# Kernel optimization log

Measured on AMD Instinct MI355X. Metric: run time of the kernel, lower is better.

Reference implementation:

```python
import jax, jax.numpy as jnp
import numpy as np


def setup_inputs() -> dict:
    key = jax.random.key(0)
    k1, k2 = jax.random.split(key)
    inputs = jax.random.normal(k1, (4, 8, 24, 24, 64), dtype=jnp.float32)
    gamma = jax.random.normal(k2, (1,), dtype=jnp.float32)
    return {"inputs": inputs, "gamma": gamma}


def reference(inputs, gamma):
    # inputs: (B, D, H, W, C); flatten spatial dims to N = D*H*W
    B, D, H, W, C = inputs.shape
    N = D * H * W
    q = inputs.reshape(B, N, C)                       # proj_query (B, N, C)
    # energy = Q @ Q^T -> (B, N, N)
    energy = jnp.einsum('bnc,bmc->bnm', q, q)
    attention = jax.nn.softmax(energy, axis=-1)       # softmax over last axis
    out = jnp.einsum('bnm,bmc->bnc', attention, q)    # (B, N, C)
    out = out.reshape(B, D, H, W, C)
    return gamma * out + inputs
```

## Files before the change

### kernel.cpp

```cpp
#include <hip/hip_runtime.h>

typedef __bf16 bf16_t;
typedef bf16_t bf16x8 __attribute__((ext_vector_type(8)));
typedef float  f32x4  __attribute__((ext_vector_type(4)));
typedef unsigned int u32;
typedef u32    u32x4  __attribute__((ext_vector_type(4)));
typedef unsigned short u16;

#define B_SZ   4
#define N_SZ   4608
#define C_SZ   64
#define KVB    32
#define QROWS  32
#define NKVT   (N_SZ / KVB)
#define NQT    (N_SZ / QROWS)
#define WV     4
#define TPW    (NKVT / WV)

__device__ __forceinline__ f32x4 mfma16(bf16x8 a, bf16x8 b, f32x4 c) {
  return __builtin_amdgcn_mfma_f32_16x16x32_bf16(a, b, c, 0, 0, 0);
}

__device__ __forceinline__ u32 pk2(float a, float b) {
  u16 ua = __builtin_bit_cast(u16, (bf16_t)a);
  u16 ub = __builtin_bit_cast(u16, (bf16_t)b);
  return (u32)ua | ((u32)ub << 16);
}

__global__ __launch_bounds__(256) void transform_k(
    const float* __restrict__ in, bf16_t* __restrict__ khi,
    bf16_t* __restrict__ klo, bf16_t* __restrict__ vt) {
  __shared__ float tile[64 * 65];
  const int bid = blockIdx.x;
  const int b  = bid / 72;
  const int n0 = (bid - b * 72) * 64;
  const int t  = threadIdx.x;
  {
    const int nl = t >> 2, c0 = (t & 3) * 16;
    const float* src = in + ((size_t)(b * N_SZ + n0 + nl)) * C_SZ + c0;
    float v[16];
    *(float4*)(v +  0) = *(const float4*)(src +  0);
    *(float4*)(v +  4) = *(const float4*)(src +  4);
    *(float4*)(v +  8) = *(const float4*)(src +  8);
    *(float4*)(v + 12) = *(const float4*)(src + 12);
    bf16x8 h8[2], l8[2];
#pragma unroll
    for (int i = 0; i < 16; ++i) {
      bf16_t h = (bf16_t)v[i];
      h8[i >> 3][i & 7] = h;
      l8[i >> 3][i & 7] = (bf16_t)(v[i] - (float)h);
      tile[nl * 65 + c0 + i] = v[i];
    }
    bf16_t* dh = khi + ((size_t)(b * N_SZ + n0 + nl)) * C_SZ + c0;
    bf16_t* dl = klo + ((size_t)(b * N_SZ + n0 + nl)) * C_SZ + c0;
    *(bf16x8*)(dh) = h8[0]; *(bf16x8*)(dh + 8) = h8[1];
    *(bf16x8*)(dl) = l8[0]; *(bf16x8*)(dl + 8) = l8[1];
  }
  __syncthreads();
  {
    const int c = t >> 2, m0 = (t & 3) * 16;
    bf16x8 o[2];
#pragma unroll
    for (int i = 0; i < 16; ++i)
      o[i >> 3][i & 7] = (bf16_t)tile[(m0 + i) * 65 + c];
    bf16_t* dst = vt + ((size_t)(b * C_SZ + c)) * N_SZ + n0 + m0;
    *(bf16x8*)(dst) = o[0]; *(bf16x8*)(dst + 8) = o[1];
  }
}

#define LOAD_TILE(KV0, KH, KL, VF)                                             \
  {                                                                            \
    _Pragma("unroll")                                                          \
    for (int ct = 0; ct < 2; ++ct)                                             \
      _Pragma("unroll")                                                        \
      for (int ks = 0; ks < 2; ++ks) {                                         \
        const size_t a = (size_t)((KV0) + ct * 16 + c15) * C_SZ + ks * 32 + g * 8; \
        KH[ct][ks] = *(const bf16x8*)(kh_b + a);                               \
        KL[ct][ks] = *(const bf16x8*)(kl_b + a);                               \
      }                                                                        \
    _Pragma("unroll")                                                          \
    for (int co = 0; co < 4; ++co)                                             \
      VF[co] = *(const bf16x8*)(vt_b + (size_t)(co * 16 + c15) * N_SZ + (KV0) + g * 8); \
  }

__global__ __launch_bounds__(256, 2) void attn_fwd(
    const float* __restrict__ in, const bf16_t* __restrict__ khi,
    const bf16_t* __restrict__ klo, const bf16_t* __restrict__ vt,
    const float* __restrict__ gamma_p, float* __restrict__ out) {
  __shared__ float obuf[256 * 36];
  __shared__ float mlbuf[4 * 2 * 2 * 16];

  const int bid0 = blockIdx.x;
  const int bid  = (bid0 & 7) * 72 + (bid0 >> 3);
  const int b  = bid / NQT;
  const int qt = bid - b * NQT;
  const int t  = threadIdx.x;
  const int w  = t >> 6, l = t & 63;
  const int c15 = l & 15, g = l >> 4;

  const bf16_t* kh_b = khi + (size_t)b * N_SZ * C_SZ;
  const bf16_t* kl_b = klo + (size_t)b * N_SZ * C_SZ;
  const bf16_t* vt_b = vt  + (size_t)b * C_SZ * N_SZ;

  bf16x8 qh[2][2], ql[2][2];
#pragma unroll
  for (int j = 0; j < 2; ++j)
#pragma unroll
    for (int ks = 0; ks < 2; ++ks) {
      const size_t a = (size_t)(qt * QROWS + j * 16 + c15) * C_SZ + ks * 32 + g * 8;
      qh[j][ks] = *(const bf16x8*)(kh_b + a);
      ql[j][ks] = *(const bf16x8*)(kl_b + a);
    }

  f32x4 acc[4][2];
#pragma unroll
  for (int co = 0; co < 4; ++co)
#pragma unroll
    for (int j = 0; j < 2; ++j)
      acc[co][j] = (f32x4){0.f, 0.f, 0.f, 0.f};
  float m_j[2] = {-3.0e38f, -3.0e38f}, l_j[2] = {0.f, 0.f};

  const int sA = ((l >> 4) & 1) * 32 + c15;
  const int sB = sA + 16;
  const bool hi_half = (l >= 32);

  bf16x8 khf[2][2], klf[2][2], vf[4];
  LOAD_TILE(w * KVB, khf, klf, vf);

  for (int it = 0; it < TPW; ++it) {
    const int itn = (it + 1 < TPW) ? it + 1 : 0;
    const int kvn = (w + itn * WV) * KVB;
    bf16x8 nkh[2][2], nkl[2][2], nvf[4];
    LOAD_TILE(kvn, nkh, nkl, nvf);

    f32x4 s[2][2];
#pragma unroll
    for (int j = 0; j < 2; ++j)
#pragma unroll
      for (int ct = 0; ct < 2; ++ct) {
        f32x4 a = (f32x4){0.f, 0.f, 0.f, 0.f};
#pragma unroll
        for (int ks = 0; ks < 2; ++ks) {
          a = mfma16(khf[ct][ks], qh[j][ks], a);
          a = mfma16(khf[ct][ks], ql[j][ks], a);
          a = mfma16(klf[ct][ks], qh[j][ks], a);
        }
        s[j][ct] = a;
      }

#pragma unroll
    for (int j = 0; j < 2; ++j) {
      float mx = fmaxf(fmaxf(fmaxf(s[j][0][0], s[j][0][1]), fmaxf(s[j][0][2], s[j][0][3])),
                       fmaxf(fmaxf(s[j][1][0], s[j][1][1]), fmaxf(s[j][1][2], s[j][1][3])));
      mx = fmaxf(mx, __shfl_xor(mx, 16, 64));
      mx = fmaxf(mx, __shfl_xor(mx, 32, 64));
      const float mn = fmaxf(m_j[j], mx);
      const float sc = __expf(m_j[j] - mn);
      m_j[j] = mn;
      float rs = 0.f;
#pragma unroll
      for (int ct = 0; ct < 2; ++ct)
#pragma unroll
        for (int r = 0; r < 4; ++r) {
          const float e = __expf(s[j][ct][r] - mn);
          s[j][ct][r] = e;
          rs += e;
        }
      rs += __shfl_xor(rs, 16, 64);
      rs += __shfl_xor(rs, 32, 64);
      l_j[j] = l_j[j] * sc + rs;
#pragma unroll
      for (int co = 0; co < 4; ++co)
        acc[co][j] *= sc;

      const u32 L0 = pk2(s[j][0][0], s[j][0][1]);
      const u32 H0 = pk2(s[j][0][2], s[j][0][3]);
      const u32 L1 = pk2(s[j][1][0], s[j][1][1]);
      const u32 H1 = pk2(s[j][1][2], s[j][1][3]);
      const u32 aL0 = (u32)__shfl((int)L0, sA, 64);
      const u32 aL1 = (u32)__shfl((int)L1, sA, 64);
      const u32 aH0 = (u32)__shfl((int)H0, sA, 64);
      const u32 aH1 = (u32)__shfl((int)H1, sA, 64);
      const u32 bL0 = (u32)__shfl((int)L0, sB, 64);
      const u32 bL1 = (u32)__shfl((int)L1, sB, 64);
      const u32 bH0 = (u32)__shfl((int)H0, sB, 64);
      const u32 bH1 = (u32)__shfl((int)H1, sB, 64);
      const u32x4 pw = (u32x4){hi_half ? aL1 : aL0,
                               hi_half ? aH1 : aH0,
                               hi_half ? bL1 : bL0,
                               hi_half ? bH1 : bH0};
      const bf16x8 pfv = __builtin_bit_cast(bf16x8, pw);
#pragma unroll
      for (int co = 0; co < 4; ++co)
        acc[co][j] = mfma16(vf[co], pfv, acc[co][j]);
    }

#pragma unroll
    for (int ct = 0; ct < 2; ++ct)
#pragma unroll
      for (int ks = 0; ks < 2; ++ks) {
        khf[ct][ks] = nkh[ct][ks];
        klf[ct][ks] = nkl[ct][ks];
      }
#pragma unroll
    for (int co = 0; co < 4; ++co)
      vf[co] = nvf[co];
  }

  float* ob = obuf + (size_t)(w * 64 + l) * 36;
#pragma unroll
  for (int co = 0; co < 4; ++co)
#pragma unroll
    for (int j = 0; j < 2; ++j)
      *(f32x4*)(ob + (co * 2 + j) * 4) = acc[co][j];
  if (g == 0) {
#pragma unroll
    for (int j = 0; j < 2; ++j) {
      mlbuf[((w * 2 + j) * 2 + 0) * 16 + c15] = m_j[j];
      mlbuf[((w * 2 + j) * 2 + 1) * 16 + c15] = l_j[j];
    }
  }
  __syncthreads();

  const float gm = gamma_p[0];
#pragma unroll
  for (int j = 0; j < 2; ++j) {
    float mw[4];
#pragma unroll
    for (int wp = 0; wp < 4; ++wp)
      mw[wp] = mlbuf[((wp * 2 + j) * 2 + 0) * 16 + c15];
    const float ms = fmaxf(fmaxf(mw[0], mw[1]), fmaxf(mw[2], mw[3]));
    float ls = 0.f;
    f32x4 mg = (f32x4){0.f, 0.f, 0.f, 0.f};
#pragma unroll
    for (int wp = 0; wp < 4; ++wp) {
      const float cf = __expf(mw[wp] - ms);
      ls += cf * mlbuf[((wp * 2 + j) * 2 + 1) * 16 + c15];
      const f32x4 pv = *(const f32x4*)(obuf + (size_t)(wp * 64 + l) * 36 + (w * 2 + j) * 4);
      mg += pv * cf;
    }
    const float inv = 1.0f / ls;
    const int q  = qt * QROWS + j * 16 + c15;
    const int cb = w * 16 + g * 4;
    const size_t base = ((size_t)(b * N_SZ + q)) * C_SZ + cb;
    const float4 iv = *(const float4*)(in + base);
    float4 ov;
    ov.x = gm * (mg[0] * inv) + iv.x;
    ov.y = gm * (mg[1] * inv) + iv.y;
    ov.z = gm * (mg[2] * inv) + iv.z;
    ov.w = gm * (mg[3] * inv) + iv.w;
    *(float4*)(out + base) = ov;
  }
}

extern "C" void kernel_launch(void* const* d_in, const int* in_sizes, int n_in,
                              void* d_out, int out_size, void* d_ws, size_t ws_size,
                              hipStream_t stream) {
  const float* in = (const float*)d_in[0];
  const float* gp = (const float*)d_in[1];
  float* op = (float*)d_out;
  const size_t plane = (size_t)B_SZ * N_SZ * C_SZ;
  bf16_t* khi = (bf16_t*)d_ws;
  bf16_t* klo = khi + plane;
  bf16_t* vt  = klo + plane;
  hipLaunchKernelGGL(transform_k, dim3(288), dim3(256), 0, stream, in, khi, klo, vt);
  hipLaunchKernelGGL(attn_fwd, dim3(B_SZ * NQT), dim3(256), 0, stream,
                     in, khi, klo, vt, gp, op);
}
```

Before: 208.9 us.

## Split KV range across blocks with combine kernel, exp2 prescale, and lazy rescale

Attention is split into four KV chunks per query tile, each handled by its own block, so the grid is four times larger. Partial outputs and row max/sum go to workspace, and a new combine kernel merges them and applies the gamma residual. Q/K are prescaled by sqrt(log2 e) so exp2 can replace exp. The running max is only updated when it grows past a threshold, which skips most accumulator rescales. The cost is an extra launch and workspace round trip, plus some added risk to numerical accuracy from the lazy-max threshold.

```diff
diff --git a/kernel.cpp b/kernel.cpp
--- a/kernel.cpp
+++ b/kernel.cpp
@@ -15,7 +15,12 @@
 #define NKVT   (N_SZ / KVB)
 #define NQT    (N_SZ / QROWS)
 #define WV     4
-#define TPW    (NKVT / WV)
+#define SPLIT  4
+#define TPC    (NKVT / SPLIT)
+#define TPW    (TPC / WV)
+#define NBLK   (B_SZ * NQT * SPLIT)
+#define RSC    1.2011224087864498f
+#define THR    11.0f
 
 __device__ __forceinline__ f32x4 mfma16(bf16x8 a, bf16x8 b, f32x4 c) {
   return __builtin_amdgcn_mfma_f32_16x16x32_bf16(a, b, c, 0, 0, 0);
@@ -46,9 +51,10 @@
     bf16x8 h8[2], l8[2];
 #pragma unroll
     for (int i = 0; i < 16; ++i) {
-      bf16_t h = (bf16_t)v[i];
+      const float vs = RSC * v[i];
+      bf16_t h = (bf16_t)vs;
       h8[i >> 3][i & 7] = h;
-      l8[i >> 3][i & 7] = (bf16_t)(v[i] - (float)h);
+      l8[i >> 3][i & 7] = (bf16_t)(vs - (float)h);
       tile[nl * 65 + c0 + i] = v[i];
     }
     bf16_t* dh = khi + ((size_t)(b * N_SZ + n0 + nl)) * C_SZ + c0;
@@ -83,17 +89,20 @@
       VF[co] = *(const bf16x8*)(vt_b + (size_t)(co * 16 + c15) * N_SZ + (KV0) + g * 8); \
   }
 
-__global__ __launch_bounds__(256, 2) void attn_fwd(
-    const float* __restrict__ in, const bf16_t* __restrict__ khi,
-    const bf16_t* __restrict__ klo, const bf16_t* __restrict__ vt,
-    const float* __restrict__ gamma_p, float* __restrict__ out) {
+__global__ __launch_bounds__(256, 2) void attn_part(
+    const bf16_t* __restrict__ khi, const bf16_t* __restrict__ klo,
+    const bf16_t* __restrict__ vt, float* __restrict__ wsO,
+    float* __restrict__ wsML) {
   __shared__ float obuf[256 * 36];
   __shared__ float mlbuf[4 * 2 * 2 * 16];
 
   const int bid0 = blockIdx.x;
-  const int bid  = (bid0 & 7) * 72 + (bid0 >> 3);
-  const int b  = bid / NQT;
-  const int qt = bid - b * NQT;
+  const int g8   = (bid0 & 7) * (NBLK / 8) + (bid0 >> 3);
+  const int b    = g8 / (NQT * SPLIT);
+  const int rem  = g8 - b * (NQT * SPLIT);
+  const int s    = rem / NQT;
+  const int qt   = rem - s * NQT;
+  const int blk  = (b * NQT + qt) * SPLIT + s;
   const int t  = threadIdx.x;
   const int w  = t >> 6, l = t & 63;
   const int c15 = l & 15, g = l >> 4;
@@ -125,15 +134,15 @@
   const bool hi_half = (l >= 32);
 
   bf16x8 khf[2][2], klf[2][2], vf[4];
-  LOAD_TILE(w * KVB, khf, klf, vf);
+  LOAD_TILE((s * TPC + w) * KVB, khf, klf, vf);
 
   for (int it = 0; it < TPW; ++it) {
     const int itn = (it + 1 < TPW) ? it + 1 : 0;
-    const int kvn = (w + itn * WV) * KVB;
+    const int kvn = (s * TPC + w + itn * WV) * KVB;
     bf16x8 nkh[2][2], nkl[2][2], nvf[4];
     LOAD_TILE(kvn, nkh, nkl, nvf);
 
-    f32x4 s[2][2];
+    f32x4 sv[2][2];
 #pragma unroll
     for (int j = 0; j < 2; ++j)
 #pragma unroll
@@ -145,38 +154,41 @@
           a = mfma16(khf[ct][ks], ql[j][ks], a);
           a = mfma16(klf[ct][ks], qh[j][ks], a);
         }
-        s[j][ct] = a;
+        sv[j][ct] = a;
       }
 
 #pragma unroll
     for (int j = 0; j < 2; ++j) {
-      float mx = fmaxf(fmaxf(fmaxf(s[j][0][0], s[j][0][1]), fmaxf(s[j][0][2], s[j][0][3])),
-                       fmaxf(fmaxf(s[j][1][0], s[j][1][1]), fmaxf(s[j][1][2], s[j][1][3])));
+      float mx = fmaxf(fmaxf(fmaxf(sv[j][0][0], sv[j][0][1]), fmaxf(sv[j][0][2], sv[j][0][3])),
+                       fmaxf(fmaxf(sv[j][1][0], sv[j][1][1]), fmaxf(sv[j][1][2], sv[j][1][3])));
       mx = fmaxf(mx, __shfl_xor(mx, 16, 64));
       mx = fmaxf(mx, __shfl_xor(mx, 32, 64));
-      const float mn = fmaxf(m_j[j], mx);
-      const float sc = __expf(m_j[j] - mn);
-      m_j[j] = mn;
+      if (__any(mx > m_j[j] + THR)) {
+        const float mn = fmaxf(m_j[j], mx);
+        const float sc = exp2f(m_j[j] - mn);
+        m_j[j] = mn;
+        l_j[j] *= sc;
+#pragma unroll
+        for (int co = 0; co < 4; ++co)
+          acc[co][j] *= sc;
+      }
       float rs = 0.f;
 #pragma unroll
       for (int ct = 0; ct < 2; ++ct)
 #pragma unroll
         for (int r = 0; r < 4; ++r) {
-          const float e = __expf(s[j][ct][r] - mn);
-          s[j][ct][r] = e;
+          const float e = exp2f(sv[j][ct][r] - m_j[j]);
+          sv[j][ct][r] = e;
           rs += e;
         }
       rs += __shfl_xor(rs, 16, 64);
       rs += __shfl_xor(rs, 32, 64);
-      l_j[j] = l_j[j] * sc + rs;
-#pragma unroll
-      for (int co = 0; co < 4; ++co)
-        acc[co][j] *= sc;
-
-      const u32 L0 = pk2(s[j][0][0], s[j][0][1]);
-      const u32 H0 = pk2(s[j][0][2], s[j][0][3]);
-      const u32 L1 = pk2(s[j][1][0], s[j][1][1]);
-      const u32 H1 = pk2(s[j][1][2], s[j][1][3]);
+      l_j[j] += rs;
+
+      const u32 L0 = pk2(sv[j][0][0], sv[j][0][1]);
+      const u32 H0 = pk2(sv[j][0][2], sv[j][0][3]);
+      const u32 L1 = pk2(sv[j][1][0], sv[j][1][1]);
+      const u32 H1 = pk2(sv[j][1][2], sv[j][1][3]);
       const u32 aL0 = (u32)__shfl((int)L0, sA, 64);
       const u32 aL1 = (u32)__shfl((int)L1, sA, 64);
       const u32 aH0 = (u32)__shfl((int)H0, sA, 64);
@@ -222,7 +234,8 @@
   }
   __syncthreads();
 
-  const float gm = gamma_p[0];
+  float* pO  = wsO  + (size_t)blk * (QROWS * C_SZ);
+  float* pML = wsML + (size_t)blk * (QROWS * 2);
 #pragma unroll
   for (int j = 0; j < 2; ++j) {
     float mw[4];
@@ -234,23 +247,67 @@
     f32x4 mg = (f32x4){0.f, 0.f, 0.f, 0.f};
 #pragma unroll
     for (int wp = 0; wp < 4; ++wp) {
-      const float cf = __expf(mw[wp] - ms);
+      const float cf = exp2f(mw[wp] - ms);
       ls += cf * mlbuf[((wp * 2 + j) * 2 + 1) * 16 + c15];
       const f32x4 pv = *(const f32x4*)(obuf + (size_t)(wp * 64 + l) * 36 + (w * 2 + j) * 4);
       mg += pv * cf;
     }
-    const float inv = 1.0f / ls;
-    const int q  = qt * QROWS + j * 16 + c15;
+    const int q  = j * 16 + c15;
     const int cb = w * 16 + g * 4;
-    const size_t base = ((size_t)(b * N_SZ + q)) * C_SZ + cb;
-    const float4 iv = *(const float4*)(in + base);
-    float4 ov;
-    ov.x = gm * (mg[0] * inv) + iv.x;
-    ov.y = gm * (mg[1] * inv) + iv.y;
-    ov.z = gm * (mg[2] * inv) + iv.z;
-    ov.w = gm * (mg[3] * inv) + iv.w;
-    *(float4*)(out + base) = ov;
-  }
+    *(f32x4*)&pO[q * C_SZ + cb] = mg;
+    if (w == 0 && g == 0) {
+      pML[q * 2 + 0] = ms;
+      pML[q * 2 + 1] = ls;
+    }
+  }
+}
+
+__global__ __launch_bounds__(256) void combine_k(
+    const float* __restrict__ in, const float* __restrict__ gamma_p,
+    const float* __restrict__ wsO, const float* __restrict__ wsML,
+    float* __restrict__ out) {
+  const int bid = blockIdx.x;
+  const int b   = bid / NQT;
+  const int qt  = bid - b * NQT;
+  const int t   = threadIdx.x;
+  const int q   = t >> 3;
+  const int c0  = (t & 7) * 8;
+  const int blk0 = bid * SPLIT;
+
+  float m[SPLIT], lv[SPLIT];
+  f32x4 o0[SPLIT], o1[SPLIT];
+#pragma unroll
+  for (int s = 0; s < SPLIT; ++s) {
+    const float* pML = wsML + (size_t)(blk0 + s) * (QROWS * 2);
+    m[s]  = pML[q * 2 + 0];
+    lv[s] = pML[q * 2 + 1];
+    const float* pO = wsO + (size_t)(blk0 + s) * (QROWS * C_SZ) + q * C_SZ + c0;
+    o0[s] = *(const f32x4*)(pO);
+    o1[s] = *(const f32x4*)(pO + 4);
+  }
+  const float ms = fmaxf(fmaxf(m[0], m[1]), fmaxf(m[2], m[3]));
+  float ls = 0.f;
+  f32x4 a0 = (f32x4){0.f, 0.f, 0.f, 0.f};
+  f32x4 a1 = (f32x4){0.f, 0.f, 0.f, 0.f};
+#pragma unroll
+  for (int s = 0; s < SPLIT; ++s) {
+    const float cf = exp2f(m[s] - ms);
+    ls += cf * lv[s];
+    a0 += o0[s] * cf;
+    a1 += o1[s] * cf;
+  }
+  const float sc = gamma_p[0] / ls;
+  const int row = qt * QROWS + q;
+  const size_t base = ((size_t)(b * N_SZ + row)) * C_SZ + c0;
+  const float4 i0 = *(const float4*)(in + base);
+  const float4 i1 = *(const float4*)(in + base + 4);
+  float4 v0, v1;
+  v0.x = a0[0] * sc + i0.x; v0.y = a0[1] * sc + i0.y;
+  v0.z = a0[2] * sc + i0.z; v0.w = a0[3] * sc + i0.w;
+  v1.x = a1[0] * sc + i1.x; v1.y = a1[1] * sc + i1.y;
+  v1.z = a1[2] * sc + i1.z; v1.w = a1[3] * sc + i1.w;
+  *(float4*)(out + base)     = v0;
+  *(float4*)(out + base + 4) = v1;
 }
 
 extern "C" void kernel_launch(void* const* d_in, const int* in_sizes, int n_in,
@@ -263,7 +320,12 @@
   bf16_t* khi = (bf16_t*)d_ws;
   bf16_t* klo = khi + plane;
   bf16_t* vt  = klo + plane;
+  float*  wsO  = (float*)((char*)d_ws + 3 * plane * sizeof(bf16_t));
+  float*  wsML = wsO + (size_t)NBLK * (QROWS * C_SZ);
+
   hipLaunchKernelGGL(transform_k, dim3(288), dim3(256), 0, stream, in, khi, klo, vt);
-  hipLaunchKernelGGL(attn_fwd, dim3(B_SZ * NQT), dim3(256), 0, stream,
-                     in, khi, klo, vt, gp, op);
-}
+  hipLaunchKernelGGL(attn_part, dim3(NBLK), dim3(256), 0, stream,
+                     khi, klo, vt, wsO, wsML);
+  hipLaunchKernelGGL(combine_k, dim3(B_SZ * NQT), dim3(256), 0, stream,
+                     in, gp, wsO, wsML, op);
+}
```

After: 187.8 us. 10.1% less time.
